# Kernel tuning notes

Measured on AMD Instinct MI355X. Metric: run time of the kernel, lower is better.

The kernel has to match this reference:

```python
import jax, jax.numpy as jnp
import numpy as np
import math

HEADS = 8
CH = 16  # hidden_channels per head
SCALE = 1.0 / math.sqrt(CH)


def _transformer_conv(x, src, dst, qw, qb, kw, kb, vw, vb, sw, sb):
    """PyG TransformerConv (concat=True, root_weight=True, eval mode -> no dropout)."""
    N = x.shape[0]
    q = (x @ qw + qb).reshape(N, HEADS, CH)
    k = (x @ kw + kb).reshape(N, HEADS, CH)
    v = (x @ vw + vb).reshape(N, HEADS, CH)
    # per-edge attention logits: message from src j to dst i
    alpha = jnp.sum(q[dst] * k[src], axis=-1) * SCALE        # [E, H]
    # segment softmax over incoming edges of each dst node
    m = jax.ops.segment_max(alpha, dst, num_segments=N)      # [N, H]
    a = jnp.exp(alpha - m[dst])                              # [E, H]
    denom = jax.ops.segment_sum(a, dst, num_segments=N)      # [N, H]
    a = a / denom[dst]
    msg = v[src] * a[:, :, None]                             # [E, H, C]
    out = jax.ops.segment_sum(msg, dst, num_segments=N).reshape(N, HEADS * CH)
    return out + x @ sw + sb  # skip connection (lin_skip)


def setup_inputs() -> dict:
    key = jax.random.key(0)
    ks = jax.random.split(key, 16)
    N, E, IN = 50000, 800000, 128
    D = HEADS * CH  # 128

    def lin(k, fi, fo):
        return (jax.random.normal(k, (fi, fo), jnp.float32) / math.sqrt(fi))

    inp = {
        "x": jax.random.normal(ks[0], (N, IN), jnp.float32),
        "edge_index": jax.random.randint(ks[1], (2, E), 0, N, dtype=jnp.int64),
        "edge_attr": jax.random.normal(ks[2], (E, 1), jnp.float32),
        # conv1: in_channels -> hidden*heads
        "q_w0": lin(ks[3], IN, D), "q_b0": jnp.zeros((D,), jnp.float32),
        "k_w0": lin(ks[4], IN, D), "k_b0": jnp.zeros((D,), jnp.float32),
        "v_w0": lin(ks[5], IN, D), "v_b0": jnp.zeros((D,), jnp.float32),
        "s_w0": lin(ks[6], IN, D), "s_b0": jnp.zeros((D,), jnp.float32),
        # conv2[0]: hidden*heads -> hidden*heads
        "q_w1": lin(ks[7], D, D), "q_b1": jnp.zeros((D,), jnp.float32),
        "k_w1": lin(ks[8], D, D), "k_b1": jnp.zeros((D,), jnp.float32),
        "v_w1": lin(ks[9], D, D), "v_b1": jnp.zeros((D,), jnp.float32),
        "s_w1": lin(ks[10], D, D), "s_b1": jnp.zeros((D,), jnp.float32),
    }
    return inp


def reference(x, edge_index, edge_attr,
              q_w0, q_b0, k_w0, k_b0, v_w0, v_b0, s_w0, s_b0,
              q_w1, q_b1, k_w1, k_b1, v_w1, v_b1, s_w1, s_b1):
    src, dst = edge_index[0], edge_index[1]
    # edge_attr is accepted but unused by the original forward
    h = _transformer_conv(x, src, dst, q_w0, q_b0, k_w0, k_b0, v_w0, v_b0, s_w0, s_b0)
    h = jax.nn.relu(h)
    h = _transformer_conv(h, src, dst, q_w1, q_b1, k_w1, k_b1, v_w1, v_b1, s_w1, s_b1)
    return h
```

## Files before the change

### kernel.cpp

```cpp
#include <hip/hip_runtime.h>
#include <math.h>


#define HEADS 8
#define CH 16
#define DM 128
#define SCALE 0.25f

typedef __attribute__((ext_vector_type(8))) short short8;
typedef __attribute__((ext_vector_type(4))) float floatx4;
typedef __attribute__((ext_vector_type(2))) float floatx2;

static __device__ __forceinline__ ushort f2bf(float f) {
    unsigned u = __float_as_uint(f);
    unsigned r = u + 0x7FFFu + ((u >> 16) & 1u);
    return (ushort)(r >> 16);
}
static __device__ __forceinline__ float bflo(unsigned u) {
    return __uint_as_float(u << 16);
}
static __device__ __forceinline__ float bfhi(unsigned u) {
    return __uint_as_float(u & 0xFFFF0000u);
}
static __device__ __forceinline__ unsigned pack2bf(float lo, float hi) {
    return (unsigned)f2bf(lo) | ((unsigned)f2bf(hi) << 16);
}
static __device__ __forceinline__ floatx2 fp8lo(unsigned v) {
    return __builtin_amdgcn_cvt_pk_f32_fp8(v, false);
}
static __device__ __forceinline__ floatx2 fp8hi(unsigned v) {
    return __builtin_amdgcn_cvt_pk_f32_fp8(v, true);
}

__global__ __launch_bounds__(256)
void cvt_wP8(const float* __restrict__ W0, const float* __restrict__ W1,
             const float* __restrict__ W2, const float* __restrict__ W3,
             const float* __restrict__ W4, const float* __restrict__ W5,
             const float* __restrict__ W6, const float* __restrict__ W7,
             ushort* __restrict__ WT)
{
    const float* Ws[8] = {W0, W1, W2, W3, W4, W5, W6, W7};
    const float* W = Ws[blockIdx.y];
    int idx = blockIdx.x * 256 + threadIdx.x;
    int c    = idx >> 9;
    int s    = idx & 511;
    int lane = s >> 3, j = s & 7;
    int w  = c >> 3, ks = (c >> 1) & 3, t = c & 1;
    int n = w * 32 + t * 16 + (lane & 15);
    int k = ks * 32 + (lane >> 4) * 8 + j;
    WT[(size_t)blockIdx.y * 16384 + idx] = f2bf(W[k * 128 + n]);
}

#define AP 136

__global__ __launch_bounds__(512)
void gemm_mfma(const float* __restrict__ Xf, const ushort* __restrict__ Xb,
               const ushort* __restrict__ WT,
               const float* __restrict__ bq, const float* __restrict__ bk,
               const float* __restrict__ bv, const float* __restrict__ bsk,
               ushort* __restrict__ Qb, ushort* __restrict__ Kb,
               unsigned char* __restrict__ Vq, ushort* __restrict__ Sb, int N)
{
    __shared__ ushort As[32 * AP];

    const int row0 = blockIdx.x * 32;
    const int tid  = threadIdx.x;

    if (Xf) {
        #pragma unroll
        for (int i = 0; i < 2; ++i) {
            int id = tid + i * 512;
            int r = id >> 5, ch = id & 31;
            float4 v = make_float4(0.f, 0.f, 0.f, 0.f);
            if (row0 + r < N)
                v = *(const float4*)(Xf + (size_t)(row0 + r) * DM + ch * 4);
            ushort4 sv;
            sv.x = f2bf(v.x); sv.y = f2bf(v.y);
            sv.z = f2bf(v.z); sv.w = f2bf(v.w);
            *(ushort4*)(As + r * AP + ch * 4) = sv;
        }
    } else {
        {
            int id = tid;
            int r = id >> 4, ch = id & 15;
            uint4 v = make_uint4(0, 0, 0, 0);
            if (row0 + r < N)
                v = *(const uint4*)(Xb + (size_t)(row0 + r) * DM + ch * 8);
            *(uint4*)(As + r * AP + ch * 8) = v;
        }
    }
    __syncthreads();

    const int lane = tid & 63, w = tid >> 6;
    const int band = w & 3;
    const int m0   = (w >> 2) * 2;
    const int lr = lane & 15, lq = lane >> 4;

    short8 a[4][2];
    #pragma unroll
    for (int ks = 0; ks < 4; ++ks) {
        const int koff = ks * 32 + lq * 8;
        #pragma unroll
        for (int mt = 0; mt < 2; ++mt)
            a[ks][mt] = *(const short8*)(As + (mt * 16 + lr) * AP + koff);
    }

    #pragma unroll
    for (int mi = 0; mi < 2; ++mi) {
        const int mat = m0 + mi;
        const ushort* Wband = WT + (size_t)mat * 16384 + (size_t)band * 4096;
        const float* bias = (mat == 0) ? bq : (mat == 1) ? bk
                          : (mat == 2) ? bv : bsk;
        floatx4 acc[2][2] = {};
        #pragma unroll
        for (int ks = 0; ks < 4; ++ks) {
            short8 b[2];
            #pragma unroll
            for (int t = 0; t < 2; ++t)
                b[t] = *(const short8*)(Wband + (ks * 2 + t) * 512 + lane * 8);
            #pragma unroll
            for (int mt = 0; mt < 2; ++mt)
                #pragma unroll
                for (int nt = 0; nt < 2; ++nt)
                    acc[mt][nt] = __builtin_amdgcn_mfma_f32_16x16x32_bf16(
                        a[ks][mt], b[nt], acc[mt][nt], 0, 0, 0);
        }
        const int nq = band * 32;
        if (mat == 2) {
            #pragma unroll
            for (int nt = 0; nt < 2; ++nt) {
                const int col = nq + nt * 16 + lr;
                const float bcol = bias[col];
                #pragma unroll
                for (int mt = 0; mt < 2; ++mt) {
                    const int rbase = row0 + mt * 16 + lq * 4;
                    #pragma unroll
                    for (int r = 0; r < 4; ++r) {
                        const int row = rbase + r;
                        if (row < N) {
                            float v = acc[mt][nt][r] + bcol;
                            unsigned p = __builtin_amdgcn_cvt_pk_fp8_f32(
                                v, v, 0u, false);
                            Vq[(size_t)row * DM + col] = (unsigned char)p;
                        }
                    }
                }
            }
        } else {
            ushort* OutB = (mat == 0) ? Qb : (mat == 1) ? Kb : Sb;
            #pragma unroll
            for (int nt = 0; nt < 2; ++nt) {
                const int col = nq + nt * 16 + lr;
                const float bcol = bias[col];
                #pragma unroll
                for (int mt = 0; mt < 2; ++mt) {
                    const int rbase = row0 + mt * 16 + lq * 4;
                    #pragma unroll
                    for (int r = 0; r < 4; ++r) {
                        const int row = rbase + r;
                        if (row < N)
                            OutB[(size_t)row * DM + col] = f2bf(acc[mt][nt][r] + bcol);
                    }
                }
            }
        }
    }
}

__global__ __launch_bounds__(256)
void hist_k(const int* __restrict__ dst, int* __restrict__ counts, int E)
{
    int e4 = (blockIdx.x * 256 + threadIdx.x) * 4;
    if (e4 + 3 < E) {
        const int4 d = *(const int4*)(dst + e4);
        atomicAdd(&counts[d.x], 1);
        atomicAdd(&counts[d.y], 1);
        atomicAdd(&counts[d.z], 1);
        atomicAdd(&counts[d.w], 1);
    } else {
        for (int e = e4; e < E; ++e) atomicAdd(&counts[dst[e]], 1);
    }
}

__global__ __launch_bounds__(256)
void scan_p1(const int* __restrict__ counts, int* __restrict__ rowptr,
             int* __restrict__ bsums, int* __restrict__ dbins, int N)
{
    __shared__ int s[256];
    __shared__ int lb[256];
    const int t = threadIdx.x;
    const int base = blockIdx.x * 1024 + t * 4;
    lb[t] = 0;
    int c[4];
    int sum = 0;
    #pragma unroll
    for (int j = 0; j < 4; ++j) {
        c[j] = (base + j < N) ? counts[base + j] : 0;
        sum += c[j];
    }
    s[t] = sum;
    __syncthreads();
    #pragma unroll
    for (int j = 0; j < 4; ++j)
        if (base + j < N) atomicAdd(&lb[min(c[j], 255)], 1);
    for (int off = 1; off < 256; off <<= 1) {
        int v = (t >= off) ? s[t - off] : 0;
        __syncthreads();
        if (t >= off) s[t] += v;
        __syncthreads();
    }
    int ex = (t == 0) ? 0 : s[t - 1];
    #pragma unroll
    for (int j = 0; j < 4; ++j) {
        if (base + j < N) rowptr[base + j] = ex;
        ex += c[j];
    }
    if (t == 255) bsums[blockIdx.x] = s[255];
    if (lb[t] > 0) atomicAdd(&dbins[t], lb[t]);
}

__global__ __launch_bounds__(256)
void scan_p2(const int* __restrict__ bsums, int* __restrict__ bbase, int nb,
             const int* __restrict__ dbins, int* __restrict__ dcur)
{
    __shared__ int s[256];
    const int t = threadIdx.x;
    s[t] = (t < nb) ? bsums[t] : 0;
    __syncthreads();
    for (int off = 1; off < 256; off <<= 1) {
        int v = (t >= off) ? s[t - off] : 0;
        __syncthreads();
        if (t >= off) s[t] += v;
        __syncthreads();
    }
    if (t <= nb) bbase[t] = (t == 0) ? 0 : s[t - 1];
    __syncthreads();
    s[t] = dbins[255 - t];
    __syncthreads();
    for (int off = 1; off < 256; off <<= 1) {
        int v = (t >= off) ? s[t - off] : 0;
        __syncthreads();
        if (t >= off) s[t] += v;
        __syncthreads();
    }
    dcur[255 - t] = (t == 0) ? 0 : s[t - 1];
}

__global__ __launch_bounds__(256)
void scan_p3(int* __restrict__ rowptr, int* __restrict__ cursor,
             const int* __restrict__ bbase, int N, int nb)
{
    int i = blockIdx.x * 256 + threadIdx.x;
    if (i < N) {
        int v = rowptr[i] + bbase[i >> 10];
        rowptr[i] = v;
        cursor[i] = v;
    }
    if (i == 0) rowptr[N] = bbase[nb];
}

__global__ __launch_bounds__(256)
void scatter_k(const int* __restrict__ src, const int* __restrict__ dst,
               int* __restrict__ cursor, int* __restrict__ esrc, int E)
{
    int e4 = (blockIdx.x * 256 + threadIdx.x) * 4;
    if (e4 + 3 < E) {
        const int4 s = *(const int4*)(src + e4);
        const int4 d = *(const int4*)(dst + e4);
        esrc[atomicAdd(&cursor[d.x], 1)] = s.x;
        esrc[atomicAdd(&cursor[d.y], 1)] = s.y;
        esrc[atomicAdd(&cursor[d.z], 1)] = s.z;
        esrc[atomicAdd(&cursor[d.w], 1)] = s.w;
    } else {
        for (int e = e4; e < E; ++e) {
            int pos = atomicAdd(&cursor[dst[e]], 1);
            esrc[pos] = src[e];
        }
    }
}

__global__ __launch_bounds__(256)
void dscatter_k(const int* __restrict__ counts, int* __restrict__ dcur,
                int* __restrict__ perm, int N)
{
    __shared__ int lc[256];
    __shared__ int lbase[256];
    const int t = threadIdx.x;
    lc[t] = 0;
    __syncthreads();
    const int n = blockIdx.x * 256 + t;
    int bin = 0, rank = 0;
    const bool valid = (n < N);
    if (valid) {
        bin = min(counts[n], 255);
        rank = atomicAdd(&lc[bin], 1);
    }
    __syncthreads();
    if (lc[t] > 0) lbase[t] = atomicAdd(&dcur[t], lc[t]);
    __syncthreads();
    if (valid) perm[lbase[bin] + rank] = n;
}

__global__ __launch_bounds__(256)
void node_attn(const ushort* __restrict__ Qb, const ushort* __restrict__ Kb,
               const unsigned char* __restrict__ Vq,
               const int* __restrict__ rowptr, const int* __restrict__ esrc,
               const int* __restrict__ perm,
               const ushort* __restrict__ Yb, float* __restrict__ Yout,
               ushort* __restrict__ Bout, int N, int relu)
{
    const int idx = blockIdx.x * 8 + (threadIdx.x >> 5);
    if (idx >= N) return;
    const int nid = perm[idx];
    const int c4 = (threadIdx.x & 31) * 4;
    const uint2 qv = *(const uint2*)(Qb + (size_t)nid * DM + c4);
    const float qx = bflo(qv.x), qy = bfhi(qv.x);
    const float qz = bflo(qv.y), qw = bfhi(qv.y);
    const int beg = rowptr[nid], end = rowptr[nid + 1];

    float lA = 0.f, lB = 0.f;
    float a0 = 0.f, a1 = 0.f, a2 = 0.f, a3 = 0.f;
    float b0 = 0.f, b1 = 0.f, b2 = 0.f, b3 = 0.f;

    int i = beg;
    for (; i + 7 < end; i += 8) {
        const int s0 = __builtin_nontemporal_load(esrc + i);
        const int s1 = __builtin_nontemporal_load(esrc + i + 1);
        const int s2 = __builtin_nontemporal_load(esrc + i + 2);
        const int s3 = __builtin_nontemporal_load(esrc + i + 3);
        const int s4 = __builtin_nontemporal_load(esrc + i + 4);
        const int s5 = __builtin_nontemporal_load(esrc + i + 5);
        const int s6 = __builtin_nontemporal_load(esrc + i + 6);
        const int s7 = __builtin_nontemporal_load(esrc + i + 7);
        const uint2 kA = *(const uint2*)(Kb + (size_t)s0 * DM + c4);
        const uint2 kB = *(const uint2*)(Kb + (size_t)s1 * DM + c4);
        const uint2 kC = *(const uint2*)(Kb + (size_t)s2 * DM + c4);
        const uint2 kD = *(const uint2*)(Kb + (size_t)s3 * DM + c4);
        const uint2 kE = *(const uint2*)(Kb + (size_t)s4 * DM + c4);
        const uint2 kF = *(const uint2*)(Kb + (size_t)s5 * DM + c4);
        const uint2 kG = *(const uint2*)(Kb + (size_t)s6 * DM + c4);
        const uint2 kH = *(const uint2*)(Kb + (size_t)s7 * DM + c4);
        const unsigned vA = *(const unsigned*)(Vq + (size_t)s0 * DM + c4);
        const unsigned vB = *(const unsigned*)(Vq + (size_t)s1 * DM + c4);
        const unsigned vC = *(const unsigned*)(Vq + (size_t)s2 * DM + c4);
        const unsigned vD = *(const unsigned*)(Vq + (size_t)s3 * DM + c4);
        const unsigned vE = *(const unsigned*)(Vq + (size_t)s4 * DM + c4);
        const unsigned vF = *(const unsigned*)(Vq + (size_t)s5 * DM + c4);
        const unsigned vG = *(const unsigned*)(Vq + (size_t)s6 * DM + c4);
        const unsigned vH = *(const unsigned*)(Vq + (size_t)s7 * DM + c4);
        float pA = qx * bflo(kA.x);
        pA = fmaf(qy, bfhi(kA.x), pA);
        pA = fmaf(qz, bflo(kA.y), pA);
        pA = fmaf(qw, bfhi(kA.y), pA);
        float pB = qx * bflo(kB.x);
        pB = fmaf(qy, bfhi(kB.x), pB);
        pB = fmaf(qz, bflo(kB.y), pB);
        pB = fmaf(qw, bfhi(kB.y), pB);
        float pC = qx * bflo(kC.x);
        pC = fmaf(qy, bfhi(kC.x), pC);
        pC = fmaf(qz, bflo(kC.y), pC);
        pC = fmaf(qw, bfhi(kC.y), pC);
        float pD = qx * bflo(kD.x);
        pD = fmaf(qy, bfhi(kD.x), pD);
        pD = fmaf(qz, bflo(kD.y), pD);
        pD = fmaf(qw, bfhi(kD.y), pD);
        float pE = qx * bflo(kE.x);
        pE = fmaf(qy, bfhi(kE.x), pE);
        pE = fmaf(qz, bflo(kE.y), pE);
        pE = fmaf(qw, bfhi(kE.y), pE);
        float pF = qx * bflo(kF.x);
        pF = fmaf(qy, bfhi(kF.x), pF);
        pF = fmaf(qz, bflo(kF.y), pF);
        pF = fmaf(qw, bfhi(kF.y), pF);
        float pG = qx * bflo(kG.x);
        pG = fmaf(qy, bfhi(kG.x), pG);
        pG = fmaf(qz, bflo(kG.y), pG);
        pG = fmaf(qw, bfhi(kG.y), pG);
        float pH = qx * bflo(kH.x);
        pH = fmaf(qy, bfhi(kH.x), pH);
        pH = fmaf(qz, bflo(kH.y), pH);
        pH = fmaf(qw, bfhi(kH.y), pH);
        pA += __shfl_xor(pA, 1, 4); pA += __shfl_xor(pA, 2, 4);
        pB += __shfl_xor(pB, 1, 4); pB += __shfl_xor(pB, 2, 4);
        pC += __shfl_xor(pC, 1, 4); pC += __shfl_xor(pC, 2, 4);
        pD += __shfl_xor(pD, 1, 4); pD += __shfl_xor(pD, 2, 4);
        pE += __shfl_xor(pE, 1, 4); pE += __shfl_xor(pE, 2, 4);
        pF += __shfl_xor(pF, 1, 4); pF += __shfl_xor(pF, 2, 4);
        pG += __shfl_xor(pG, 1, 4); pG += __shfl_xor(pG, 2, 4);
        pH += __shfl_xor(pH, 1, 4); pH += __shfl_xor(pH, 2, 4);
        const float wA = __expf(pA * SCALE);
        const float wB = __expf(pB * SCALE);
        const float wC = __expf(pC * SCALE);
        const float wD = __expf(pD * SCALE);
        const float wE = __expf(pE * SCALE);
        const float wF = __expf(pF * SCALE);
        const float wG = __expf(pG * SCALE);
        const float wH = __expf(pH * SCALE);
        lA += (wA + wC) + (wE + wG);
        lB += (wB + wD) + (wF + wH);
        {
            const floatx2 dA0 = fp8lo(vA), dA1 = fp8hi(vA);
            const floatx2 dB0 = fp8lo(vB), dB1 = fp8hi(vB);
            a0 = fmaf(wA, dA0.x, a0); b0 = fmaf(wB, dB0.x, b0);
            a1 = fmaf(wA, dA0.y, a1); b1 = fmaf(wB, dB0.y, b1);
            a2 = fmaf(wA, dA1.x, a2); b2 = fmaf(wB, dB1.x, b2);
            a3 = fmaf(wA, dA1.y, a3); b3 = fmaf(wB, dB1.y, b3);
        }
        {
            const floatx2 dC0 = fp8lo(vC), dC1 = fp8hi(vC);
            const floatx2 dD0 = fp8lo(vD), dD1 = fp8hi(vD);
            a0 = fmaf(wC, dC0.x, a0); b0 = fmaf(wD, dD0.x, b0);
            a1 = fmaf(wC, dC0.y, a1); b1 = fmaf(wD, dD0.y, b1);
            a2 = fmaf(wC, dC1.x, a2); b2 = fmaf(wD, dD1.x, b2);
            a3 = fmaf(wC, dC1.y, a3); b3 = fmaf(wD, dD1.y, b3);
        }
        {
            const floatx2 dE0 = fp8lo(vE), dE1 = fp8hi(vE);
            const floatx2 dF0 = fp8lo(vF), dF1 = fp8hi(vF);
            a0 = fmaf(wE, dE0.x, a0); b0 = fmaf(wF, dF0.x, b0);
            a1 = fmaf(wE, dE0.y, a1); b1 = fmaf(wF, dF0.y, b1);
            a2 = fmaf(wE, dE1.x, a2); b2 = fmaf(wF, dF1.x, b2);
            a3 = fmaf(wE, dE1.y, a3); b3 = fmaf(wF, dF1.y, b3);
        }
        {
            const floatx2 dG0 = fp8lo(vG), dG1 = fp8hi(vG);
            const floatx2 dH0 = fp8lo(vH), dH1 = fp8hi(vH);
            a0 = fmaf(wG, dG0.x, a0); b0 = fmaf(wH, dH0.x, b0);
            a1 = fmaf(wG, dG0.y, a1); b1 = fmaf(wH, dH0.y, b1);
            a2 = fmaf(wG, dG1.x, a2); b2 = fmaf(wH, dH1.x, b2);
            a3 = fmaf(wG, dG1.y, a3); b3 = fmaf(wH, dH1.y, b3);
        }
    }
    for (; i + 3 < end; i += 4) {
        const int s0 = __builtin_nontemporal_load(esrc + i);
        const int s1 = __builtin_nontemporal_load(esrc + i + 1);
        const int s2 = __builtin_nontemporal_load(esrc + i + 2);
        const int s3 = __builtin_nontemporal_load(esrc + i + 3);
        const uint2 kA = *(const uint2*)(Kb + (size_t)s0 * DM + c4);
        const uint2 kB = *(const uint2*)(Kb + (size_t)s1 * DM + c4);
        const uint2 kC = *(const uint2*)(Kb + (size_t)s2 * DM + c4);
        const uint2 kD = *(const uint2*)(Kb + (size_t)s3 * DM + c4);
        const unsigned vA = *(const unsigned*)(Vq + (size_t)s0 * DM + c4);
        const unsigned vB = *(const unsigned*)(Vq + (size_t)s1 * DM + c4);
        const unsigned vC = *(const unsigned*)(Vq + (size_t)s2 * DM + c4);
        const unsigned vD = *(const unsigned*)(Vq + (size_t)s3 * DM + c4);
        float pA = qx * bflo(kA.x);
        pA = fmaf(qy, bfhi(kA.x), pA);
        pA = fmaf(qz, bflo(kA.y), pA);
        pA = fmaf(qw, bfhi(kA.y), pA);
        float pB = qx * bflo(kB.x);
        pB = fmaf(qy, bfhi(kB.x), pB);
        pB = fmaf(qz, bflo(kB.y), pB);
        pB = fmaf(qw, bfhi(kB.y), pB);
        float pC = qx * bflo(kC.x);
        pC = fmaf(qy, bfhi(kC.x), pC);
        pC = fmaf(qz, bflo(kC.y), pC);
        pC = fmaf(qw, bfhi(kC.y), pC);
        float pD = qx * bflo(kD.x);
        pD = fmaf(qy, bfhi(kD.x), pD);
        pD = fmaf(qz, bflo(kD.y), pD);
        pD = fmaf(qw, bfhi(kD.y), pD);
        pA += __shfl_xor(pA, 1, 4); pA += __shfl_xor(pA, 2, 4);
        pB += __shfl_xor(pB, 1, 4); pB += __shfl_xor(pB, 2, 4);
        pC += __shfl_xor(pC, 1, 4); pC += __shfl_xor(pC, 2, 4);
        pD += __shfl_xor(pD, 1, 4); pD += __shfl_xor(pD, 2, 4);
        const float wA = __expf(pA * SCALE);
        const float wB = __expf(pB * SCALE);
        const float wC = __expf(pC * SCALE);
        const float wD = __expf(pD * SCALE);
        lA += wA + wC;
        lB += wB + wD;
        {
            const floatx2 dA0 = fp8lo(vA), dA1 = fp8hi(vA);
            const floatx2 dB0 = fp8lo(vB), dB1 = fp8hi(vB);
            a0 = fmaf(wA, dA0.x, a0); b0 = fmaf(wB, dB0.x, b0);
            a1 = fmaf(wA, dA0.y, a1); b1 = fmaf(wB, dB0.y, b1);
            a2 = fmaf(wA, dA1.x, a2); b2 = fmaf(wB, dB1.x, b2);
            a3 = fmaf(wA, dA1.y, a3); b3 = fmaf(wB, dB1.y, b3);
        }
        {
            const floatx2 dC0 = fp8lo(vC), dC1 = fp8hi(vC);
            const floatx2 dD0 = fp8lo(vD), dD1 = fp8hi(vD);
            a0 = fmaf(wC, dC0.x, a0); b0 = fmaf(wD, dD0.x, b0);
            a1 = fmaf(wC, dC0.y, a1); b1 = fmaf(wD, dD0.y, b1);
            a2 = fmaf(wC, dC1.x, a2); b2 = fmaf(wD, dD1.x, b2);
            a3 = fmaf(wC, dC1.y, a3); b3 = fmaf(wD, dD1.y, b3);
        }
    }
    for (; i < end; ++i) {
        const int s0 = __builtin_nontemporal_load(esrc + i);
        const uint2 kA = *(const uint2*)(Kb + (size_t)s0 * DM + c4);
        const unsigned vA = *(const unsigned*)(Vq + (size_t)s0 * DM + c4);
        float p = qx * bflo(kA.x);
        p = fmaf(qy, bfhi(kA.x), p);
        p = fmaf(qz, bflo(kA.y), p);
        p = fmaf(qw, bfhi(kA.y), p);
        p += __shfl_xor(p, 1, 4);
        p += __shfl_xor(p, 2, 4);
        const float wg = __expf(p * SCALE);
        lA += wg;
        const floatx2 dA0 = fp8lo(vA), dA1 = fp8hi(vA);
        a0 = fmaf(wg, dA0.x, a0);
        a1 = fmaf(wg, dA0.y, a1);
        a2 = fmaf(wg, dA1.x, a2);
        a3 = fmaf(wg, dA1.y, a3);
    }
    const float l = lA + lB;
    a0 += b0; a1 += b1; a2 += b2; a3 += b3;

    const float inv = (l > 0.f) ? 1.f / l : 0.f;
    const uint2 yb = *(const uint2*)(Yb + (size_t)nid * DM + c4);
    float y0 = fmaf(a0, inv, bflo(yb.x));
    float y1 = fmaf(a1, inv, bfhi(yb.x));
    float y2 = fmaf(a2, inv, bflo(yb.y));
    float y3 = fmaf(a3, inv, bfhi(yb.y));
    if (relu) {
        y0 = fmaxf(y0, 0.f); y1 = fmaxf(y1, 0.f);
        y2 = fmaxf(y2, 0.f); y3 = fmaxf(y3, 0.f);
    }
    if (Yout) {
        float4 o = make_float4(y0, y1, y2, y3);
        *(float4*)(Yout + (size_t)nid * DM + c4) = o;
    }
    if (Bout) {
        uint2 o;
        o.x = pack2bf(y0, y1);
        o.y = pack2bf(y2, y3);
        *(uint2*)(Bout + (size_t)nid * DM + c4) = o;
    }
}

extern "C" void kernel_launch(void* const* d_in, const int* in_sizes, int n_in,
                              void* d_out, int out_size, void* d_ws, size_t ws_size,
                              hipStream_t stream)
{
    const float* x   = (const float*)d_in[0];
    const int* eidx  = (const int*)d_in[1];
    const float* qw0 = (const float*)d_in[3];  const float* qb0 = (const float*)d_in[4];
    const float* kw0 = (const float*)d_in[5];  const float* kb0 = (const float*)d_in[6];
    const float* vw0 = (const float*)d_in[7];  const float* vb0 = (const float*)d_in[8];
    const float* sw0 = (const float*)d_in[9];  const float* sb0 = (const float*)d_in[10];
    const float* qw1 = (const float*)d_in[11]; const float* qb1 = (const float*)d_in[12];
    const float* kw1 = (const float*)d_in[13]; const float* kb1 = (const float*)d_in[14];
    const float* vw1 = (const float*)d_in[15]; const float* vb1 = (const float*)d_in[16];
    const float* sw1 = (const float*)d_in[17]; const float* sb1 = (const float*)d_in[18];

    const int N = in_sizes[0] / DM;
    const int E = in_sizes[1] / 2;
    const int* src = eidx;
    const int* dst = eidx + E;

    size_t nd  = (size_t)N * DM;
    ushort* Qb = (ushort*)d_ws;
    ushort* Kb = Qb + nd;
    ushort* Xb = Kb + nd;
    ushort* Sb = Xb + nd;
    ushort* WT = Sb + nd;
    unsigned char* Vq = (unsigned char*)(WT + 8 * 16384);
    int* counts = (int*)(Vq + nd);
    int* rowptr = counts + N;
    int* cursor = rowptr + (N + 1);
    int* esrc   = cursor + N;
    int* perm   = esrc + E;
    int* dbins  = perm + N;
    int* dcur   = dbins + 256;
    int* bsums  = dcur + 256;
    int* bbase  = bsums + 256;
    float* out  = (float*)d_out;

    const int nb = (N + 1023) / 1024;
    hipMemsetAsync(counts, 0, (size_t)N * sizeof(int), stream);
    hipMemsetAsync(dbins, 0, 256 * sizeof(int), stream);
    hist_k<<<(E + 1023) / 1024, 256, 0, stream>>>(dst, counts, E);
    scan_p1<<<nb, 256, 0, stream>>>(counts, rowptr, bsums, dbins, N);
    scan_p2<<<1, 256, 0, stream>>>(bsums, bbase, nb, dbins, dcur);
    scan_p3<<<(N + 255) / 256, 256, 0, stream>>>(rowptr, cursor, bbase, N, nb);
    scatter_k<<<(E + 1023) / 1024, 256, 0, stream>>>(src, dst, cursor, esrc, E);
    dscatter_k<<<(N + 255) / 256, 256, 0, stream>>>(counts, dcur, perm, N);

    const int ggrid = (N + 31) / 32;
    const int ablk = (N + 7) / 8;

    cvt_wP8<<<dim3(64, 8), 256, 0, stream>>>(qw0, kw0, vw0, sw0,
                                             qw1, kw1, vw1, sw1, WT);

    gemm_mfma<<<ggrid, 512, 0, stream>>>(x, nullptr, WT, qb0, kb0, vb0, sb0,
                                         Qb, Kb, Vq, Sb, N);
    node_attn<<<ablk, 256, 0, stream>>>(Qb, Kb, Vq, rowptr, esrc, perm,
                                        Sb, nullptr, Xb, N, 1);

    gemm_mfma<<<ggrid, 512, 0, stream>>>(nullptr, Xb, WT + 4 * 16384,
                                         qb1, kb1, vb1, sb1,
                                         Qb, Kb, Vq, Sb, N);
    node_attn<<<ablk, 256, 0, stream>>>(Qb, Kb, Vq, rowptr, esrc, perm,
                                        Sb, out, nullptr, N, 0);
}
```

Baseline: 359.5 us.

## Merge weight conversion with histogram and scatter kernels with first GEMM

Folds the weight bf16 conversion into the degree-histogram launch, and merges the edge scatter, degree-bucket permutation and first-layer QKV/skip GEMM into one heterogeneous launch, with blocks dispatched by index range. This cuts the launch count and lets the independent GEMM blocks overlap the atomic-heavy CSR build instead of running back to back. The scatter and permutation parts now run with 512-thread blocks, and all branches share the GEMM's shared-memory footprint and 512-thread launch bounds.

```diff
diff --git a/kernel.cpp b/kernel.cpp
--- a/kernel.cpp
+++ b/kernel.cpp
@@ -32,38 +32,18 @@
     return __builtin_amdgcn_cvt_pk_f32_fp8(v, true);
 }
 
-__global__ __launch_bounds__(256)
-void cvt_wP8(const float* __restrict__ W0, const float* __restrict__ W1,
-             const float* __restrict__ W2, const float* __restrict__ W3,
-             const float* __restrict__ W4, const float* __restrict__ W5,
-             const float* __restrict__ W6, const float* __restrict__ W7,
-             ushort* __restrict__ WT)
-{
-    const float* Ws[8] = {W0, W1, W2, W3, W4, W5, W6, W7};
-    const float* W = Ws[blockIdx.y];
-    int idx = blockIdx.x * 256 + threadIdx.x;
-    int c    = idx >> 9;
-    int s    = idx & 511;
-    int lane = s >> 3, j = s & 7;
-    int w  = c >> 3, ks = (c >> 1) & 3, t = c & 1;
-    int n = w * 32 + t * 16 + (lane & 15);
-    int k = ks * 32 + (lane >> 4) * 8 + j;
-    WT[(size_t)blockIdx.y * 16384 + idx] = f2bf(W[k * 128 + n]);
-}
-
 #define AP 136
 
-__global__ __launch_bounds__(512)
-void gemm_mfma(const float* __restrict__ Xf, const ushort* __restrict__ Xb,
-               const ushort* __restrict__ WT,
-               const float* __restrict__ bq, const float* __restrict__ bk,
-               const float* __restrict__ bv, const float* __restrict__ bsk,
-               ushort* __restrict__ Qb, ushort* __restrict__ Kb,
-               unsigned char* __restrict__ Vq, ushort* __restrict__ Sb, int N)
-{
-    __shared__ ushort As[32 * AP];
-
-    const int row0 = blockIdx.x * 32;
+static __device__ __forceinline__ void gemm_body(
+    int bx, const float* __restrict__ Xf, const ushort* __restrict__ Xb,
+    const ushort* __restrict__ WT,
+    const float* __restrict__ bq, const float* __restrict__ bk,
+    const float* __restrict__ bv, const float* __restrict__ bsk,
+    ushort* __restrict__ Qb, ushort* __restrict__ Kb,
+    unsigned char* __restrict__ Vq, ushort* __restrict__ Sb, int N,
+    ushort* As)
+{
+    const int row0 = bx * 32;
     const int tid  = threadIdx.x;
 
     if (Xf) {
@@ -80,14 +60,12 @@
             *(ushort4*)(As + r * AP + ch * 4) = sv;
         }
     } else {
-        {
-            int id = tid;
-            int r = id >> 4, ch = id & 15;
-            uint4 v = make_uint4(0, 0, 0, 0);
-            if (row0 + r < N)
-                v = *(const uint4*)(Xb + (size_t)(row0 + r) * DM + ch * 8);
-            *(uint4*)(As + r * AP + ch * 8) = v;
-        }
+        int id = tid;
+        int r = id >> 4, ch = id & 15;
+        uint4 v = make_uint4(0, 0, 0, 0);
+        if (row0 + r < N)
+            v = *(const uint4*)(Xb + (size_t)(row0 + r) * DM + ch * 8);
+        *(uint4*)(As + r * AP + ch * 8) = v;
     }
     __syncthreads();
 
@@ -168,17 +146,36 @@
 }
 
 __global__ __launch_bounds__(256)
-void hist_k(const int* __restrict__ dst, int* __restrict__ counts, int E)
-{
-    int e4 = (blockIdx.x * 256 + threadIdx.x) * 4;
-    if (e4 + 3 < E) {
-        const int4 d = *(const int4*)(dst + e4);
-        atomicAdd(&counts[d.x], 1);
-        atomicAdd(&counts[d.y], 1);
-        atomicAdd(&counts[d.z], 1);
-        atomicAdd(&counts[d.w], 1);
+void cvt_hist(const float* __restrict__ W0, const float* __restrict__ W1,
+              const float* __restrict__ W2, const float* __restrict__ W3,
+              const float* __restrict__ W4, const float* __restrict__ W5,
+              const float* __restrict__ W6, const float* __restrict__ W7,
+              ushort* __restrict__ WT,
+              const int* __restrict__ dst, int* __restrict__ counts, int E)
+{
+    const int b = blockIdx.x;
+    if (b < 512) {
+        const float* Ws[8] = {W0, W1, W2, W3, W4, W5, W6, W7};
+        const float* W = Ws[b >> 6];
+        int idx = (b & 63) * 256 + threadIdx.x;
+        int c    = idx >> 9;
+        int s    = idx & 511;
+        int lane = s >> 3, j = s & 7;
+        int w  = c >> 3, ks = (c >> 1) & 3, t = c & 1;
+        int n = w * 32 + t * 16 + (lane & 15);
+        int k = ks * 32 + (lane >> 4) * 8 + j;
+        WT[(size_t)(b >> 6) * 16384 + idx] = f2bf(W[k * 128 + n]);
     } else {
-        for (int e = e4; e < E; ++e) atomicAdd(&counts[dst[e]], 1);
+        int e4 = ((b - 512) * 256 + threadIdx.x) * 4;
+        if (e4 + 3 < E) {
+            const int4 d = *(const int4*)(dst + e4);
+            atomicAdd(&counts[d.x], 1);
+            atomicAdd(&counts[d.y], 1);
+            atomicAdd(&counts[d.z], 1);
+            atomicAdd(&counts[d.w], 1);
+        } else {
+            for (int e = e4; e < E; ++e) atomicAdd(&counts[dst[e]], 1);
+        }
     }
 }
 
@@ -259,46 +256,69 @@
     if (i == 0) rowptr[N] = bbase[nb];
 }
 
-__global__ __launch_bounds__(256)
-void scatter_k(const int* __restrict__ src, const int* __restrict__ dst,
-               int* __restrict__ cursor, int* __restrict__ esrc, int E)
-{
-    int e4 = (blockIdx.x * 256 + threadIdx.x) * 4;
-    if (e4 + 3 < E) {
-        const int4 s = *(const int4*)(src + e4);
-        const int4 d = *(const int4*)(dst + e4);
-        esrc[atomicAdd(&cursor[d.x], 1)] = s.x;
-        esrc[atomicAdd(&cursor[d.y], 1)] = s.y;
-        esrc[atomicAdd(&cursor[d.z], 1)] = s.z;
-        esrc[atomicAdd(&cursor[d.w], 1)] = s.w;
-    } else {
-        for (int e = e4; e < E; ++e) {
-            int pos = atomicAdd(&cursor[dst[e]], 1);
-            esrc[pos] = src[e];
-        }
-    }
-}
-
-__global__ __launch_bounds__(256)
-void dscatter_k(const int* __restrict__ counts, int* __restrict__ dcur,
-                int* __restrict__ perm, int N)
-{
+__global__ __launch_bounds__(512)
+void gemm_scat(const float* __restrict__ Xf, const ushort* __restrict__ Xb,
+               const ushort* __restrict__ WT,
+               const float* __restrict__ bq, const float* __restrict__ bk,
+               const float* __restrict__ bv, const float* __restrict__ bsk,
+               ushort* __restrict__ Qb, ushort* __restrict__ Kb,
+               unsigned char* __restrict__ Vq, ushort* __restrict__ Sb, int N,
+               const int* __restrict__ src, const int* __restrict__ dst,
+               int* __restrict__ cursor, int* __restrict__ esrc,
+               const int* __restrict__ counts, int* __restrict__ dcur,
+               int* __restrict__ perm, int E, int sb, int db)
+{
+    __shared__ ushort As[32 * AP];
     __shared__ int lc[256];
     __shared__ int lbase[256];
-    const int t = threadIdx.x;
-    lc[t] = 0;
-    __syncthreads();
-    const int n = blockIdx.x * 256 + t;
-    int bin = 0, rank = 0;
-    const bool valid = (n < N);
-    if (valid) {
-        bin = min(counts[n], 255);
-        rank = atomicAdd(&lc[bin], 1);
-    }
-    __syncthreads();
-    if (lc[t] > 0) lbase[t] = atomicAdd(&dcur[t], lc[t]);
-    __syncthreads();
-    if (valid) perm[lbase[bin] + rank] = n;
+
+    const int b = blockIdx.x;
+    if (b < sb) {
+        int e4 = (b * 512 + (int)threadIdx.x) * 4;
+        if (e4 + 3 < E) {
+            const int4 s = *(const int4*)(src + e4);
+            const int4 d = *(const int4*)(dst + e4);
+            esrc[atomicAdd(&cursor[d.x], 1)] = s.x;
+            esrc[atomicAdd(&cursor[d.y], 1)] = s.y;
+            esrc[atomicAdd(&cursor[d.z], 1)] = s.z;
+            esrc[atomicAdd(&cursor[d.w], 1)] = s.w;
+        } else {
+            for (int e = e4; e < E; ++e) {
+                int pos = atomicAdd(&cursor[dst[e]], 1);
+                esrc[pos] = src[e];
+            }
+        }
+    } else if (b < sb + db) {
+        const int t = threadIdx.x;
+        if (t < 256) lc[t] = 0;
+        __syncthreads();
+        const int n = (b - sb) * 512 + t;
+        int bin = 0, rank = 0;
+        const bool valid = (n < N);
+        if (valid) {
+            bin = min(counts[n], 255);
+            rank = atomicAdd(&lc[bin], 1);
+        }
+        __syncthreads();
+        if (t < 256 && lc[t] > 0) lbase[t] = atomicAdd(&dcur[t], lc[t]);
+        __syncthreads();
+        if (valid) perm[lbase[bin] + rank] = n;
+    } else {
+        gemm_body(b - sb - db, Xf, Xb, WT, bq, bk, bv, bsk,
+                  Qb, Kb, Vq, Sb, N, As);
+    }
+}
+
+__global__ __launch_bounds__(512)
+void gemm_mfma(const float* __restrict__ Xf, const ushort* __restrict__ Xb,
+               const ushort* __restrict__ WT,
+               const float* __restrict__ bq, const float* __restrict__ bk,
+               const float* __restrict__ bv, const float* __restrict__ bsk,
+               ushort* __restrict__ Qb, ushort* __restrict__ Kb,
+               unsigned char* __restrict__ Vq, ushort* __restrict__ Sb, int N)
+{
+    __shared__ ushort As[32 * AP];
+    gemm_body(blockIdx.x, Xf, Xb, WT, bq, bk, bv, bsk, Qb, Kb, Vq, Sb, N, As);
 }
 
 __global__ __launch_bounds__(256)
@@ -569,23 +589,25 @@
     float* out  = (float*)d_out;
 
     const int nb = (N + 1023) / 1024;
+    const int ggrid = (N + 31) / 32;
+    const int ablk = (N + 7) / 8;
+    const int sb = (E + 2047) / 2048;
+    const int db = (N + 511) / 512;
+
     hipMemsetAsync(counts, 0, (size_t)N * sizeof(int), stream);
     hipMemsetAsync(dbins, 0, 256 * sizeof(int), stream);
-    hist_k<<<(E + 1023) / 1024, 256, 0, stream>>>(dst, counts, E);
+
+    cvt_hist<<<512 + (E + 1023) / 1024, 256, 0, stream>>>(
+        qw0, kw0, vw0, sw0, qw1, kw1, vw1, sw1, WT, dst, counts, E);
+
     scan_p1<<<nb, 256, 0, stream>>>(counts, rowptr, bsums, dbins, N);
     scan_p2<<<1, 256, 0, stream>>>(bsums, bbase, nb, dbins, dcur);
     scan_p3<<<(N + 255) / 256, 256, 0, stream>>>(rowptr, cursor, bbase, N, nb);
-    scatter_k<<<(E + 1023) / 1024, 256, 0, stream>>>(src, dst, cursor, esrc, E);
-    dscatter_k<<<(N + 255) / 256, 256, 0, stream>>>(counts, dcur, perm, N);
-
-    const int ggrid = (N + 31) / 32;
-    const int ablk = (N + 7) / 8;
-
-    cvt_wP8<<<dim3(64, 8), 256, 0, stream>>>(qw0, kw0, vw0, sw0,
-                                             qw1, kw1, vw1, sw1, WT);
-
-    gemm_mfma<<<ggrid, 512, 0, stream>>>(x, nullptr, WT, qb0, kb0, vb0, sb0,
-                                         Qb, Kb, Vq, Sb, N);
+
+    gemm_scat<<<sb + db + ggrid, 512, 0, stream>>>(
+        x, nullptr, WT, qb0, kb0, vb0, sb0, Qb, Kb, Vq, Sb, N,
+        src, dst, cursor, esrc, counts, dcur, perm, E, sb, db);
+
     node_attn<<<ablk, 256, 0, stream>>>(Qb, Kb, Vq, rowptr, esrc, perm,
                                         Sb, nullptr, Xb, N, 1);
 
```

New measurement: 344.8 us, median of 2. 1.04x faster.
